# Performance work log

Hardware: AMD Instinct MI355X
Metric: run time of the kernel (lower is better)

Reference implementation:

```python
import jax, jax.numpy as jnp
import numpy as np

N_QUBITS = 4


def _apply_ry(state, theta, wire):
    """Apply RY(theta) on `wire`. state: (B,2,2,2,2) real; theta: (B,) or scalar."""
    ax = wire + 1
    half = theta * 0.5
    c, s = jnp.cos(half), jnp.sin(half)
    a0 = jax.lax.index_in_dim(state, 0, axis=ax, keepdims=False)
    a1 = jax.lax.index_in_dim(state, 1, axis=ax, keepdims=False)
    if c.ndim:  # per-sample angles -> broadcast over remaining qubit axes
        c = c.reshape((-1,) + (1,) * (a0.ndim - 1))
        s = s.reshape((-1,) + (1,) * (a0.ndim - 1))
    n0 = c * a0 - s * a1
    n1 = s * a0 + c * a1
    return jnp.stack([n0, n1], axis=ax)


def _apply_cnot(state, control, target):
    """CNOT on the (B,2,2,2,2) statevector: flip target where control==1."""
    cax = control + 1
    s0 = jax.lax.index_in_dim(state, 0, axis=cax, keepdims=False)
    s1 = jax.lax.index_in_dim(state, 1, axis=cax, keepdims=False)
    # after removing the control axis, axes after it shift down by one
    tax = target + 1 if target < control else target
    s1 = jnp.flip(s1, axis=tax)
    return jnp.stack([s0, s1], axis=cax)


def _circuit(x, weights):
    """Batched 4-qubit circuit. x: (B,4) angles; weights: (3,4). Returns (B,4) <Z_i>."""
    B = x.shape[0]
    state = jnp.zeros((B, 2, 2, 2, 2), dtype=x.dtype).at[:, 0, 0, 0, 0].set(1.0)
    for i in range(N_QUBITS):
        state = _apply_ry(state, x[:, i], i)
    for layer in range(3):
        for i in range(N_QUBITS):
            state = _apply_ry(state, weights[layer, i], i)
        if layer < 2:  # CNOT ring between RY layers
            for i in range(3):
                state = _apply_cnot(state, i, i + 1)
            state = _apply_cnot(state, 3, 0)
    probs = state * state  # real statevector -> |amp|^2
    expvals = []
    for w in range(N_QUBITS):
        other = tuple(a for a in range(1, N_QUBITS + 1) if a != w + 1)
        p = probs.sum(axis=other)  # (B,2)
        expvals.append(p[:, 0] - p[:, 1])
    return jnp.stack(expvals, axis=1)  # (B,4)


def setup_inputs() -> dict:
    key = jax.random.key(0)
    k1, k2, k3, k4 = jax.random.split(key, 4)
    B = 1_000_000
    return {
        "x": jax.random.normal(k1, (B, 4), dtype=jnp.float32),
        "quantum_weights": jax.random.normal(k2, (3, 4), dtype=jnp.float32),
        "W": jax.random.normal(k3, (6, 4), dtype=jnp.float32) * 0.5,
        "b": jax.random.normal(k4, (6,), dtype=jnp.float32) * 0.1,
    }


def reference(x, quantum_weights, W, b):
    q_out = _circuit(x, quantum_weights)          # (B,4)
    logits = q_out @ W.T + b                      # Linear(4,6)
    return jax.nn.softmax(logits, axis=1)         # (B,6)
```

## Files before the change

### kernel.cpp

```cpp
#include <hip/hip_runtime.h>


#define INV_2PI 0.15915494309189535f

template <int MASK>
__device__ __forceinline__ void apply_ry(float st[16], float c, float s) {
#pragma unroll
    for (int i = 0; i < 16; ++i) {
        if (!(i & MASK)) {
            float a0 = st[i];
            float a1 = st[i | MASK];
            st[i]        = fmaf(c, a0, -s * a1);
            st[i | MASK] = fmaf(s, a0,  c * a1);
        }
    }
}

template <int CMASK, int TMASK>
__device__ __forceinline__ void apply_cnot(float st[16]) {
#pragma unroll
    for (int i = 0; i < 16; ++i) {
        if ((i & CMASK) && !(i & TMASK)) {
            float tmp     = st[i];
            st[i]         = st[i | TMASK];
            st[i | TMASK] = tmp;
        }
    }
}

__global__ __launch_bounds__(256) void qnn_kernel(
    const float* __restrict__ x,
    const float* __restrict__ qw,
    const float* __restrict__ W,
    const float* __restrict__ bias,
    float* __restrict__ out,
    int B)
{
    __shared__ float qw0[4];
    __shared__ float c1h[4], s1h[4];
    __shared__ float c2f[4], s2f[4];
    __shared__ float sW[24], sb[6];
    __shared__ float so[256 * 6];

    const int tid = threadIdx.x;
    if (tid < 4) {
        qw0[tid] = qw[tid];
        float r1 = qw[4 + tid] * (0.5f * INV_2PI);
        c1h[tid] = __builtin_amdgcn_cosf(r1);
        s1h[tid] = __builtin_amdgcn_sinf(r1);
        float r2 = qw[8 + tid] * INV_2PI;
        c2f[tid] = __builtin_amdgcn_cosf(r2);
        s2f[tid] = __builtin_amdgcn_sinf(r2);
    }
    if (tid < 24) sW[tid] = W[tid];
    if (tid < 6)  sb[tid] = bias[tid];
    __syncthreads();

    const int b = blockIdx.x * 256 + tid;
    const bool valid = (b < B);

    float4 xv = valid ? reinterpret_cast<const float4*>(x)[b]
                      : make_float4(0.f, 0.f, 0.f, 0.f);

    float c0, s0, c1, s1, c2, s2, c3, s3;
    {
        float r0 = (xv.x + qw0[0]) * (0.5f * INV_2PI);
        float r1 = (xv.y + qw0[1]) * (0.5f * INV_2PI);
        float r2 = (xv.z + qw0[2]) * (0.5f * INV_2PI);
        float r3 = (xv.w + qw0[3]) * (0.5f * INV_2PI);
        c0 = __builtin_amdgcn_cosf(r0); s0 = __builtin_amdgcn_sinf(r0);
        c1 = __builtin_amdgcn_cosf(r1); s1 = __builtin_amdgcn_sinf(r1);
        c2 = __builtin_amdgcn_cosf(r2); s2 = __builtin_amdgcn_sinf(r2);
        c3 = __builtin_amdgcn_cosf(r3); s3 = __builtin_amdgcn_sinf(r3);
    }

    float a01[4] = { c0 * c1, c0 * s1, s0 * c1, s0 * s1 };
    float a23[4] = { c2 * c3, c2 * s3, s2 * c3, s2 * s3 };

    float st[16];
#pragma unroll
    for (int hi = 0; hi < 4; ++hi)
#pragma unroll
        for (int lo = 0; lo < 4; ++lo)
            st[hi * 4 + lo] = a01[hi] * a23[lo];

    apply_cnot<8, 4>(st); apply_cnot<4, 2>(st);
    apply_cnot<2, 1>(st); apply_cnot<1, 8>(st);

    apply_ry<8>(st, c1h[0], s1h[0]);
    apply_ry<4>(st, c1h[1], s1h[1]);
    apply_ry<2>(st, c1h[2], s1h[2]);
    apply_ry<1>(st, c1h[3], s1h[3]);

    apply_cnot<8, 4>(st); apply_cnot<4, 2>(st);
    apply_cnot<2, 1>(st); apply_cnot<1, 8>(st);

    float p[16];
#pragma unroll
    for (int i = 0; i < 16; ++i) p[i] = st[i] * st[i];

    float z[4];
#pragma unroll
    for (int w = 0; w < 4; ++w) {
        const int m = 8 >> w;
        float A1 = 0.0f, X = 0.0f;
#pragma unroll
        for (int i = 0; i < 16; ++i) {
            if (!(i & m)) {
                A1 += p[i | m];
                X  = fmaf(st[i], st[i | m], X);
            }
        }
        z[w] = fmaf(c2f[w], fmaf(-2.0f, A1, 1.0f), -2.0f * s2f[w] * X);
    }

    float e[6];
    float sum = 0.0f;
#pragma unroll
    for (int j = 0; j < 6; ++j) {
        float a = sb[j];
        a = fmaf(z[0], sW[j * 4 + 0], a);
        a = fmaf(z[1], sW[j * 4 + 1], a);
        a = fmaf(z[2], sW[j * 4 + 2], a);
        a = fmaf(z[3], sW[j * 4 + 3], a);
        e[j] = __expf(a);
        sum += e[j];
    }
    const float inv = __builtin_amdgcn_rcpf(sum);

#pragma unroll
    for (int j = 0; j < 6; ++j) so[tid * 6 + j] = e[j] * inv;
    __syncthreads();

    const float4* so4 = reinterpret_cast<const float4*>(so);
    float4* out4 = reinterpret_cast<float4*>(out);
    const long long base = (long long)blockIdx.x * 384;
    const long long total4 = (long long)B * 6 / 4;
#pragma unroll
    for (int k = 0; k < 2; ++k) {
        int idx = tid + k * 256;
        if (idx < 384 && base + idx < total4)
            out4[base + idx] = so4[idx];
    }
}

extern "C" void kernel_launch(void* const* d_in, const int* in_sizes, int n_in,
                              void* d_out, int out_size, void* d_ws, size_t ws_size,
                              hipStream_t stream) {
    const float* x    = (const float*)d_in[0];
    const float* qw   = (const float*)d_in[1];
    const float* W    = (const float*)d_in[2];
    const float* bias = (const float*)d_in[3];
    float* out = (float*)d_out;

    const int B = in_sizes[0] / 4;
    const int blocks = (B + 255) / 256;
    qnn_kernel<<<blocks, 256, 0, stream>>>(x, qw, W, bias, out, B);
}
```

Measured before the change: 81.08 us.

## Process two samples per thread and store outputs directly as float4

Each thread now computes two batch samples and writes their 12 outputs as three float4 stores straight to global memory. This removes the shared-memory staging buffer and the second __syncthreads used to coalesce output writes, and halves the block count. The cost is strided, less coalesced per-thread loads and stores (48-byte stride per thread) and higher register pressure from two unrolled statevectors per thread.

```diff
diff --git a/kernel.cpp b/kernel.cpp
--- a/kernel.cpp
+++ b/kernel.cpp
@@ -28,46 +28,20 @@
     }
 }
 
-__global__ __launch_bounds__(256) void qnn_kernel(
-    const float* __restrict__ x,
-    const float* __restrict__ qw,
-    const float* __restrict__ W,
-    const float* __restrict__ bias,
-    float* __restrict__ out,
-    int B)
+__device__ __forceinline__ void run_sample(
+    float x0, float x1, float x2, float x3,
+    const float* __restrict__ qw0,
+    const float* __restrict__ c1h, const float* __restrict__ s1h,
+    const float* __restrict__ c2f, const float* __restrict__ s2f,
+    const float* __restrict__ sW,  const float* __restrict__ sb,
+    float o[6])
 {
-    __shared__ float qw0[4];
-    __shared__ float c1h[4], s1h[4];
-    __shared__ float c2f[4], s2f[4];
-    __shared__ float sW[24], sb[6];
-    __shared__ float so[256 * 6];
-
-    const int tid = threadIdx.x;
-    if (tid < 4) {
-        qw0[tid] = qw[tid];
-        float r1 = qw[4 + tid] * (0.5f * INV_2PI);
-        c1h[tid] = __builtin_amdgcn_cosf(r1);
-        s1h[tid] = __builtin_amdgcn_sinf(r1);
-        float r2 = qw[8 + tid] * INV_2PI;
-        c2f[tid] = __builtin_amdgcn_cosf(r2);
-        s2f[tid] = __builtin_amdgcn_sinf(r2);
-    }
-    if (tid < 24) sW[tid] = W[tid];
-    if (tid < 6)  sb[tid] = bias[tid];
-    __syncthreads();
-
-    const int b = blockIdx.x * 256 + tid;
-    const bool valid = (b < B);
-
-    float4 xv = valid ? reinterpret_cast<const float4*>(x)[b]
-                      : make_float4(0.f, 0.f, 0.f, 0.f);
-
     float c0, s0, c1, s1, c2, s2, c3, s3;
     {
-        float r0 = (xv.x + qw0[0]) * (0.5f * INV_2PI);
-        float r1 = (xv.y + qw0[1]) * (0.5f * INV_2PI);
-        float r2 = (xv.z + qw0[2]) * (0.5f * INV_2PI);
-        float r3 = (xv.w + qw0[3]) * (0.5f * INV_2PI);
+        float r0 = (x0 + qw0[0]) * (0.5f * INV_2PI);
+        float r1 = (x1 + qw0[1]) * (0.5f * INV_2PI);
+        float r2 = (x2 + qw0[2]) * (0.5f * INV_2PI);
+        float r3 = (x3 + qw0[3]) * (0.5f * INV_2PI);
         c0 = __builtin_amdgcn_cosf(r0); s0 = __builtin_amdgcn_sinf(r0);
         c1 = __builtin_amdgcn_cosf(r1); s1 = __builtin_amdgcn_sinf(r1);
         c2 = __builtin_amdgcn_cosf(r2); s2 = __builtin_amdgcn_sinf(r2);
@@ -127,20 +101,57 @@
         sum += e[j];
     }
     const float inv = __builtin_amdgcn_rcpf(sum);
+#pragma unroll
+    for (int j = 0; j < 6; ++j) o[j] = e[j] * inv;
+}
 
-#pragma unroll
-    for (int j = 0; j < 6; ++j) so[tid * 6 + j] = e[j] * inv;
+__global__ __launch_bounds__(256) void qnn_kernel(
+    const float* __restrict__ x,
+    const float* __restrict__ qw,
+    const float* __restrict__ W,
+    const float* __restrict__ bias,
+    float* __restrict__ out,
+    int B)
+{
+    __shared__ float qw0[4], c1h[4], s1h[4], c2f[4], s2f[4], sW[24], sb[6];
+
+    const int tid = threadIdx.x;
+    if (tid < 4) {
+        qw0[tid] = qw[tid];
+        float r1 = qw[4 + tid] * (0.5f * INV_2PI);
+        c1h[tid] = __builtin_amdgcn_cosf(r1);
+        s1h[tid] = __builtin_amdgcn_sinf(r1);
+        float r2 = qw[8 + tid] * INV_2PI;
+        c2f[tid] = __builtin_amdgcn_cosf(r2);
+        s2f[tid] = __builtin_amdgcn_sinf(r2);
+    }
+    if (tid < 24) sW[tid] = W[tid];
+    if (tid < 6)  sb[tid] = bias[tid];
     __syncthreads();
 
-    const float4* so4 = reinterpret_cast<const float4*>(so);
-    float4* out4 = reinterpret_cast<float4*>(out);
-    const long long base = (long long)blockIdx.x * 384;
-    const long long total4 = (long long)B * 6 / 4;
+    const size_t t  = (size_t)blockIdx.x * 256u + (size_t)tid;
+    const size_t s0 = 2u * t;
+    if (s0 < (size_t)B) {
+        const float4* x4 = reinterpret_cast<const float4*>(x);
+        if (s0 + 1 < (size_t)B) {
+            float4 xa = x4[s0];
+            float4 xb = x4[s0 + 1];
+            float oa[6], ob[6];
+            run_sample(xa.x, xa.y, xa.z, xa.w, qw0, c1h, s1h, c2f, s2f, sW, sb, oa);
+            run_sample(xb.x, xb.y, xb.z, xb.w, qw0, c1h, s1h, c2f, s2f, sW, sb, ob);
+
+            float* op = out + s0 * 6u;
+            reinterpret_cast<float4*>(op)[0] = make_float4(oa[0], oa[1], oa[2], oa[3]);
+            reinterpret_cast<float4*>(op)[1] = make_float4(oa[4], oa[5], ob[0], ob[1]);
+            reinterpret_cast<float4*>(op)[2] = make_float4(ob[2], ob[3], ob[4], ob[5]);
+        } else {
+            float4 xa = x4[s0];
+            float oa[6];
+            run_sample(xa.x, xa.y, xa.z, xa.w, qw0, c1h, s1h, c2f, s2f, sW, sb, oa);
+            float* op = out + s0 * 6u;
 #pragma unroll
-    for (int k = 0; k < 2; ++k) {
-        int idx = tid + k * 256;
-        if (idx < 384 && base + idx < total4)
-            out4[base + idx] = so4[idx];
+            for (int j = 0; j < 6; ++j) op[j] = oa[j];
+        }
     }
 }
 
@@ -154,6 +165,7 @@
     float* out = (float*)d_out;
 
     const int B = in_sizes[0] / 4;
-    const int blocks = (B + 255) / 256;
+    const int threads = (B + 1) / 2;
+    const int blocks = (threads + 255) / 256;
     qnn_kernel<<<blocks, 256, 0, stream>>>(x, qw, W, bias, out, B);
 }
```

Measured after the change: 82.08 us. Within noise of the previous version (+1.2%).
